# Performance work log

Measured on AMD Instinct MI355X. Metric: run time of the kernel, lower is better.

Reference implementation:

```python
import jax, jax.numpy as jnp
import numpy as np

OUTPUT_SIZE = (32, 32, 32)
TRUNCATION = (24, 24, 24)


def dct_matrix(N):
    # Orthonormal DCT-II matrix M with y_k = sum_n M[k, n] * x_n.
    n = jnp.arange(N, dtype=jnp.float32)
    k = n[:, None]
    M = jnp.cos(jnp.pi * (n[None, :] + 0.5) * k / N)
    scale = jnp.where(n == 0, jnp.sqrt(1.0 / N), jnp.sqrt(2.0 / N))
    return M * scale[:, None]


def setup_inputs() -> dict:
    key = jax.random.key(0)
    x = jax.random.normal(key, (4, 64, 64, 64, 32), dtype=jnp.float32)
    return {"x": x}


def reference(x) -> jnp.ndarray:
    # x: [B, D, H, W, C]
    B, D, H, W, C = x.shape
    t0, t1, t2 = TRUNCATION
    o0, o1, o2 = OUTPUT_SIZE

    # 3D DCT-II (ortho), separable per spatial axis.
    Md, Mh, Mw = dct_matrix(D), dct_matrix(H), dct_matrix(W)
    y = jnp.einsum('pd,bdhwc->bphwc', Md, x)
    y = jnp.einsum('qh,bphwc->bpqwc', Mh, y)
    y = jnp.einsum('rw,bpqwc->bpqrc', Mw, y)

    # Crop low frequencies, zero-pad to output size.
    y = y[:, :t0, :t1, :t2, :]
    y = jnp.pad(y, ((0, 0), (0, o0 - t0), (0, o1 - t1), (0, o2 - t2), (0, 0)))

    # 3D inverse DCT (ortho inverse = transpose of DCT matrix).
    I0, I1, I2 = dct_matrix(o0).T, dct_matrix(o1).T, dct_matrix(o2).T
    z = jnp.einsum('dp,bpqrc->bdqrc', I0, y)
    z = jnp.einsum('hq,bdqrc->bdhrc', I1, z)
    z = jnp.einsum('wr,bdhrc->bdhwc', I2, z)

    # Original module's _idct3D permutes (0,4,3,2,1) then back, which reverses
    # the spatial axis order of the output: out[b, w, h, d, c].
    return jnp.transpose(z, (0, 3, 2, 1, 4))
```

## Files before the change

kernel.cpp:

```cpp
#include <hip/hip_runtime.h>


#define PI_D 3.14159265358979323846

__global__ __launch_bounds__(256) void sp_compute_A(float* __restrict__ A) {
    int idx = blockIdx.x * 256 + threadIdx.x;
    if (idx >= 2048) return;
    int o = idx >> 6;
    int i = idx & 63;
    double acc = 0.0;
    for (int p = 0; p < 24; ++p) {
        double s32 = (p == 0) ? sqrt(1.0 / 32.0) : sqrt(2.0 / 32.0);
        double s64 = (p == 0) ? sqrt(1.0 / 64.0) : sqrt(2.0 / 64.0);
        acc += s32 * cos(PI_D * (o + 0.5) * p / 32.0)
             * s64 * cos(PI_D * (i + 0.5) * p / 64.0);
    }
    A[idx] = (float)acc;
}

template<int PASS>
__global__ __launch_bounds__(256) void sp_pass(const float* __restrict__ X,
                                               const float* __restrict__ Amat,
                                               float* __restrict__ Y) {
    __shared__ float As[2048];
    __shared__ float tiles[4][2048];

    int t = threadIdx.x;
    for (int i = t; i < 2048; i += 256) {
        int k = i >> 5, o = i & 31;
        As[i] = Amat[o * 64 + k];
    }
    __syncthreads();

    int wave = t >> 6, lane = t & 63;
    long tile = (long)blockIdx.x * 4 + wave;

    constexpr int KS = (PASS == 1) ? 32 : (PASS == 2) ? 1024 : 32768;
    constexpr int OS = (PASS == 1) ? 32 : (PASS == 2) ? 1024 : 32;

    long in_base, out_base;
    if constexpr (PASS == 1) {
        in_base  = tile * 2048;
        out_base = tile * 1024;
    } else if constexpr (PASS == 2) {
        long bd = tile >> 5; int jt = (int)tile & 31;
        in_base  = bd * 65536 + jt * 32;
        out_base = bd * 32768 + jt * 32;
    } else {
        long b = tile >> 10; int q = ((int)tile >> 5) & 31, r = (int)tile & 31;
        in_base  = b * 2097152 + q * 1024 + r * 32;
        out_base = b * 1048576 + r * 32768 + q * 1024;
    }

    float* ltile = &tiles[wave][0];
    const float* gsrc = X + in_base + (long)(lane >> 3) * KS + (lane & 7) * 4;
#pragma unroll
    for (int i = 0; i < 8; ++i) {
        __builtin_amdgcn_global_load_lds(
            (const __attribute__((address_space(1))) void*)(gsrc + (long)i * 8 * KS),
            (__attribute__((address_space(3))) void*)(ltile + i * 256),
            16, 0, 0);
    }
    asm volatile("s_waitcnt vmcnt(0)" ::: "memory");
    __builtin_amdgcn_sched_barrier(0);

    int j2 = lane & 15, og = lane >> 4;
    const float2* xs  = (const float2*)ltile + j2;
    const float4* as4 = (const float4*)As + og * 2;

    float2 acc[8];
#pragma unroll
    for (int i = 0; i < 8; ++i) acc[i] = make_float2(0.f, 0.f);

#pragma unroll
    for (int k = 0; k < 64; ++k) {
        float2 xv = xs[k * 16];
        float4 a0 = as4[k * 8];
        float4 a1 = as4[k * 8 + 1];
        acc[0].x += a0.x * xv.x; acc[0].y += a0.x * xv.y;
        acc[1].x += a0.y * xv.x; acc[1].y += a0.y * xv.y;
        acc[2].x += a0.z * xv.x; acc[2].y += a0.z * xv.y;
        acc[3].x += a0.w * xv.x; acc[3].y += a0.w * xv.y;
        acc[4].x += a1.x * xv.x; acc[4].y += a1.x * xv.y;
        acc[5].x += a1.y * xv.x; acc[5].y += a1.y * xv.y;
        acc[6].x += a1.z * xv.x; acc[6].y += a1.z * xv.y;
        acc[7].x += a1.w * xv.x; acc[7].y += a1.w * xv.y;
    }

    float2* dst = (float2*)(Y + out_base) + j2;
#pragma unroll
    for (int i = 0; i < 8; ++i) {
        int o = og * 8 + i;
        dst[(long)o * (OS / 2)] = acc[i];
    }
}

extern "C" void kernel_launch(void* const* d_in, const int* in_sizes, int n_in,
                              void* d_out, int out_size, void* d_ws, size_t ws_size,
                              hipStream_t stream) {
    const float* x = (const float*)d_in[0];
    float* out = (float*)d_out;

    float* A  = (float*)d_ws;
    float* y1 = A + 2048;
    float* y2 = y1 + 16777216;

    sp_compute_A<<<8, 256, 0, stream>>>(A);

    sp_pass<1><<<4096, 256, 0, stream>>>(x, A, y1);

    sp_pass<2><<<2048, 256, 0, stream>>>(y1, A, y2);

    sp_pass<3><<<1024, 256, 0, stream>>>(y2, A, out);
}
```

Baseline: 253.4 us.

## Double-buffer persistent tiles per wave, compute DCT matrix inline, change pass layouts

Each wave now handles several tiles, with async global-to-LDS loads double-buffered so the next tile's load overlaps the current tile's compute. The combined truncation matrix is computed in each block with cosf, which removes the separate setup kernel. The pass-2 and pass-3 index mappings are rearranged so pass-3 reads contiguously, and the register tile becomes 4x4 with float4 stores. This adds redundant per-block trig work and slightly different numerics from single-precision cos.

```diff
diff --git a/kernel.cpp b/kernel.cpp
--- a/kernel.cpp
+++ b/kernel.cpp
@@ -1,97 +1,110 @@
 #include <hip/hip_runtime.h>
 
 
-#define PI_D 3.14159265358979323846
+template<int PASS> struct Cfg;
+template<> struct Cfg<1> { static constexpr int KS = 32;   static constexpr int NT = 8; static constexpr long OS = 32;    };
+template<> struct Cfg<2> { static constexpr int KS = 1024; static constexpr int NT = 4; static constexpr long OS = 65536; };
+template<> struct Cfg<3> { static constexpr int KS = 1024; static constexpr int NT = 2; static constexpr long OS = 32;    };
 
-__global__ __launch_bounds__(256) void sp_compute_A(float* __restrict__ A) {
-    int idx = blockIdx.x * 256 + threadIdx.x;
-    if (idx >= 2048) return;
-    int o = idx >> 6;
-    int i = idx & 63;
-    double acc = 0.0;
-    for (int p = 0; p < 24; ++p) {
-        double s32 = (p == 0) ? sqrt(1.0 / 32.0) : sqrt(2.0 / 32.0);
-        double s64 = (p == 0) ? sqrt(1.0 / 64.0) : sqrt(2.0 / 64.0);
-        acc += s32 * cos(PI_D * (o + 0.5) * p / 32.0)
-             * s64 * cos(PI_D * (i + 0.5) * p / 64.0);
+template<int PASS>
+__device__ __forceinline__ void tile_bases(long tau, long& ib, long& ob) {
+    if constexpr (PASS == 1) {
+        ib = tau * 2048;
+        ob = tau * 1024;
+    } else if constexpr (PASS == 2) {
+        long bd = tau >> 5, jt = tau & 31;
+        long b = bd >> 6, d = bd & 63;
+        ib = bd * 65536 + jt * 32;
+        ob = b * 2097152 + d * 1024 + jt * 32;
+    } else {
+        long bq = tau >> 5, jt = tau & 31;
+        long b = bq >> 5, q = bq & 31;
+        ib = (b * 32 + q) * 65536 + jt * 32;
+        ob = ((b * 32 + jt) * 32 + q) * 1024;
     }
-    A[idx] = (float)acc;
 }
 
 template<int PASS>
 __global__ __launch_bounds__(256) void sp_pass(const float* __restrict__ X,
-                                               const float* __restrict__ Amat,
                                                float* __restrict__ Y) {
+    constexpr int  KS = Cfg<PASS>::KS;
+    constexpr long OS = Cfg<PASS>::OS;
+    constexpr int  NT = Cfg<PASS>::NT;
+
     __shared__ float As[2048];
-    __shared__ float tiles[4][2048];
+    __shared__ float tiles[4][2][2048];
 
     int t = threadIdx.x;
     for (int i = t; i < 2048; i += 256) {
         int k = i >> 5, o = i & 31;
-        As[i] = Amat[o * 64 + k];
+        float fo = (o + 0.5f) * (3.14159265358979f / 32.0f);
+        float fk = (k + 0.5f) * (3.14159265358979f / 64.0f);
+        float s = 0.02209708691f;
+        for (int p = 1; p < 24; ++p)
+            s += 0.04419417382f * cosf(fo * p) * cosf(fk * p);
+        As[i] = s;
     }
     __syncthreads();
 
     int wave = t >> 6, lane = t & 63;
-    long tile = (long)blockIdx.x * 4 + wave;
+    int o4 = lane >> 3, c4 = lane & 7;
+    long wg = (long)blockIdx.x * 4 + wave;
 
-    constexpr int KS = (PASS == 1) ? 32 : (PASS == 2) ? 1024 : 32768;
-    constexpr int OS = (PASS == 1) ? 32 : (PASS == 2) ? 1024 : 32;
+    float* b0 = &tiles[wave][0][0];
+    float* b1 = &tiles[wave][1][0];
 
-    long in_base, out_base;
-    if constexpr (PASS == 1) {
-        in_base  = tile * 2048;
-        out_base = tile * 1024;
-    } else if constexpr (PASS == 2) {
-        long bd = tile >> 5; int jt = (int)tile & 31;
-        in_base  = bd * 65536 + jt * 32;
-        out_base = bd * 32768 + jt * 32;
-    } else {
-        long b = tile >> 10; int q = ((int)tile >> 5) & 31, r = (int)tile & 31;
-        in_base  = b * 2097152 + q * 1024 + r * 32;
-        out_base = b * 1048576 + r * 32768 + q * 1024;
-    }
+    const float* Xl = X + (long)(lane >> 3) * KS + (lane & 7) * 4;
+    auto issue = [&](float* buf, long ib) {
+        const float* g = Xl + ib;
+#pragma unroll
+        for (int i = 0; i < 8; ++i)
+            __builtin_amdgcn_global_load_lds(
+                (const __attribute__((address_space(1))) void*)(g + (long)i * (8 * KS)),
+                (__attribute__((address_space(3))) void*)(buf + i * 256), 16, 0, 0);
+    };
 
-    float* ltile = &tiles[wave][0];
-    const float* gsrc = X + in_base + (long)(lane >> 3) * KS + (lane & 7) * 4;
+    long ib, ob;
+    tile_bases<PASS>(wg * NT + 0, ib, ob); issue(b0, ib);
+    tile_bases<PASS>(wg * NT + 1, ib, ob); issue(b1, ib);
+
+    const float4* ab = (const float4*)As;
+
+#pragma unroll 1
+    for (int i = 0; i < NT; ++i) {
+        if (i == 0)           asm volatile("s_waitcnt vmcnt(8)"  ::: "memory");
+        else if (i == NT - 1) asm volatile("s_waitcnt vmcnt(4)"  ::: "memory");
+        else                  asm volatile("s_waitcnt vmcnt(12)" ::: "memory");
+        __builtin_amdgcn_sched_barrier(0);
+
+        const float4* tb = (const float4*)((i & 1) ? b1 : b0);
+
+        float4 a0 = make_float4(0.f, 0.f, 0.f, 0.f);
+        float4 a1 = a0, a2 = a0, a3 = a0;
 #pragma unroll
-    for (int i = 0; i < 8; ++i) {
-        __builtin_amdgcn_global_load_lds(
-            (const __attribute__((address_space(1))) void*)(gsrc + (long)i * 8 * KS),
-            (__attribute__((address_space(3))) void*)(ltile + i * 256),
-            16, 0, 0);
-    }
-    asm volatile("s_waitcnt vmcnt(0)" ::: "memory");
-    __builtin_amdgcn_sched_barrier(0);
+        for (int k = 0; k < 64; ++k) {
+            float4 xv = tb[k * 8 + c4];
+            float4 av = ab[k * 8 + o4];
+            a0.x += av.x * xv.x; a0.y += av.x * xv.y; a0.z += av.x * xv.z; a0.w += av.x * xv.w;
+            a1.x += av.y * xv.x; a1.y += av.y * xv.y; a1.z += av.y * xv.z; a1.w += av.y * xv.w;
+            a2.x += av.z * xv.x; a2.y += av.z * xv.y; a2.z += av.z * xv.z; a2.w += av.z * xv.w;
+            a3.x += av.w * xv.x; a3.y += av.w * xv.y; a3.z += av.w * xv.z; a3.w += av.w * xv.w;
+        }
 
-    int j2 = lane & 15, og = lane >> 4;
-    const float2* xs  = (const float2*)ltile + j2;
-    const float4* as4 = (const float4*)As + og * 2;
+        asm volatile("s_waitcnt lgkmcnt(0)" ::: "memory");
+        __builtin_amdgcn_sched_barrier(0);
+        if (i + 2 < NT) {
+            long ibn, obn;
+            tile_bases<PASS>(wg * NT + i + 2, ibn, obn);
+            issue((i & 1) ? b1 : b0, ibn);
+        }
 
-    float2 acc[8];
-#pragma unroll
-    for (int i = 0; i < 8; ++i) acc[i] = make_float2(0.f, 0.f);
-
-#pragma unroll
-    for (int k = 0; k < 64; ++k) {
-        float2 xv = xs[k * 16];
-        float4 a0 = as4[k * 8];
-        float4 a1 = as4[k * 8 + 1];
-        acc[0].x += a0.x * xv.x; acc[0].y += a0.x * xv.y;
-        acc[1].x += a0.y * xv.x; acc[1].y += a0.y * xv.y;
-        acc[2].x += a0.z * xv.x; acc[2].y += a0.z * xv.y;
-        acc[3].x += a0.w * xv.x; acc[3].y += a0.w * xv.y;
-        acc[4].x += a1.x * xv.x; acc[4].y += a1.x * xv.y;
-        acc[5].x += a1.y * xv.x; acc[5].y += a1.y * xv.y;
-        acc[6].x += a1.z * xv.x; acc[6].y += a1.z * xv.y;
-        acc[7].x += a1.w * xv.x; acc[7].y += a1.w * xv.y;
-    }
-
-    float2* dst = (float2*)(Y + out_base) + j2;
-#pragma unroll
-    for (int i = 0; i < 8; ++i) {
-        int o = og * 8 + i;
-        dst[(long)o * (OS / 2)] = acc[i];
+        long ibc, obc;
+        tile_bases<PASS>(wg * NT + i, ibc, obc);
+        float* dst = Y + obc + (long)(o4 * 4) * OS + c4 * 4;
+        *(float4*)(dst)          = a0;
+        *(float4*)(dst + OS)     = a1;
+        *(float4*)(dst + 2 * OS) = a2;
+        *(float4*)(dst + 3 * OS) = a3;
     }
 }
 
@@ -101,15 +114,10 @@
     const float* x = (const float*)d_in[0];
     float* out = (float*)d_out;
 
-    float* A  = (float*)d_ws;
-    float* y1 = A + 2048;
+    float* y1 = (float*)d_ws;
     float* y2 = y1 + 16777216;
 
-    sp_compute_A<<<8, 256, 0, stream>>>(A);
-
-    sp_pass<1><<<4096, 256, 0, stream>>>(x, A, y1);
-
-    sp_pass<2><<<2048, 256, 0, stream>>>(y1, A, y2);
-
-    sp_pass<3><<<1024, 256, 0, stream>>>(y2, A, out);
+    sp_pass<1><<<512, 256, 0, stream>>>(x,  y1);
+    sp_pass<2><<<512, 256, 0, stream>>>(y1, y2);
+    sp_pass<3><<<512, 256, 0, stream>>>(y2, out);
 }
```

New measurement: 441.2 us. 74.1% more time.

## Fuse W and H DCT passes into one kernel and compute matrix in-kernel

Applied to the files above, without the earlier changes.

Replaces the three separable passes plus the matrix-generation kernel with two kernels. The first streams each (b,d) slab row by row through a triple-buffered LDS pipeline and applies both the W and H transforms while keeping the H accumulators in registers. The second applies the D transform as before. The combined DCT/IDCT matrix is now built per block with a Chebyshev cosine recurrence, dropping the separate launch and one full intermediate round-trip through global memory. In exchange only 256 large blocks run in the fused pass, so parallelism is lower and register pressure is high (64 matrix values plus 32 float2 accumulators per thread).

```diff
diff --git a/kernel.cpp b/kernel.cpp
--- a/kernel.cpp
+++ b/kernel.cpp
@@ -1,66 +1,111 @@
 #include <hip/hip_runtime.h>
 
 
-#define PI_D 3.14159265358979323846
-
-__global__ __launch_bounds__(256) void sp_compute_A(float* __restrict__ A) {
-    int idx = blockIdx.x * 256 + threadIdx.x;
-    if (idx >= 2048) return;
-    int o = idx >> 6;
-    int i = idx & 63;
-    double acc = 0.0;
-    for (int p = 0; p < 24; ++p) {
-        double s32 = (p == 0) ? sqrt(1.0 / 32.0) : sqrt(2.0 / 32.0);
-        double s64 = (p == 0) ? sqrt(1.0 / 64.0) : sqrt(2.0 / 64.0);
-        acc += s32 * cos(PI_D * (o + 0.5) * p / 32.0)
-             * s64 * cos(PI_D * (i + 0.5) * p / 64.0);
+__device__ __forceinline__ void fill_As(float* As) {
+    for (int i = threadIdx.x; i < 2048; i += blockDim.x) {
+        int k = i >> 5, o = i & 31;
+        double to = cos((o + 0.5) * (3.14159265358979323846 / 32.0));
+        double tk = cos((k + 0.5) * (3.14159265358979323846 / 64.0));
+        double co0 = 1.0, co1 = to, ck0 = 1.0, ck1 = tk;
+        double w2o = 2.0 * to, w2k = 2.0 * tk;
+        double s = 0.022097086912079608;
+        #pragma unroll 1
+        for (int p = 1; p < 24; ++p) {
+            s += 0.044194173824159216 * co1 * ck1;
+            double con = w2o * co1 - co0; co0 = co1; co1 = con;
+            double ckn = w2k * ck1 - ck0; ck0 = ck1; ck1 = ckn;
+        }
+        As[i] = (float)s;
     }
-    A[idx] = (float)acc;
 }
 
-template<int PASS>
-__global__ __launch_bounds__(256) void sp_pass(const float* __restrict__ X,
-                                               const float* __restrict__ Amat,
-                                               float* __restrict__ Y) {
+__global__ __launch_bounds__(512, 2) void sp_fuse_wh(const float* __restrict__ X,
+                                                     float* __restrict__ Y1) {
+    __shared__ float As[2048];
+    __shared__ float xrow[4][2048];
+
+    int t = threadIdx.x;
+    int b = blockIdx.x >> 6, d = blockIdx.x & 63;
+    const float* xbase = X + ((long)(b * 64 + d) << 17);
+
+    auto stage = [&](int h) {
+        const float* src = xbase + h * 2048 + t * 4;
+        float* dstb = &xrow[h & 3][(t >> 6) << 8];
+        __builtin_amdgcn_global_load_lds(
+            (const __attribute__((address_space(1))) void*)src,
+            (__attribute__((address_space(3))) void*)dstb, 16, 0, 0);
+    };
+
+    stage(0); stage(1); stage(2);
+    fill_As(As);
+    __syncthreads();
+
+    int r = t >> 4;
+    int c2 = t & 15;
+
+    float ar[64];
+#pragma unroll
+    for (int w = 0; w < 64; ++w) ar[w] = As[w * 32 + r];
+
+    float2 qa[32];
+#pragma unroll
+    for (int q = 0; q < 32; ++q) qa[q] = make_float2(0.f, 0.f);
+
+#pragma unroll 1
+    for (int h = 0; h < 64; ++h) {
+        if (h < 61) asm volatile("s_waitcnt vmcnt(2)" ::: "memory");
+        else        asm volatile("s_waitcnt vmcnt(0)" ::: "memory");
+        __syncthreads();
+        if (h + 3 < 64) stage(h + 3);
+
+        const float* xr = &xrow[h & 3][0];
+        float2 v = make_float2(0.f, 0.f);
+#pragma unroll
+        for (int w = 0; w < 64; ++w) {
+            float2 xv = *(const float2*)&xr[w * 32 + c2 * 2];
+            v.x += ar[w] * xv.x; v.y += ar[w] * xv.y;
+        }
+
+        const float4* ah = (const float4*)&As[h * 32];
+#pragma unroll
+        for (int qg = 0; qg < 8; ++qg) {
+            float4 a4 = ah[qg];
+            qa[qg * 4 + 0].x += a4.x * v.x; qa[qg * 4 + 0].y += a4.x * v.y;
+            qa[qg * 4 + 1].x += a4.y * v.x; qa[qg * 4 + 1].y += a4.y * v.y;
+            qa[qg * 4 + 2].x += a4.z * v.x; qa[qg * 4 + 2].y += a4.z * v.y;
+            qa[qg * 4 + 3].x += a4.w * v.x; qa[qg * 4 + 3].y += a4.w * v.y;
+        }
+    }
+
+#pragma unroll
+    for (int q = 0; q < 32; ++q) {
+        float* dst = Y1 + ((long)((b * 32 + q) * 64 + d) << 10) + r * 32 + c2 * 2;
+        *(float2*)dst = qa[q];
+    }
+}
+
+__global__ __launch_bounds__(256) void sp_pass_d(const float* __restrict__ Y1,
+                                                 float* __restrict__ Out) {
     __shared__ float As[2048];
     __shared__ float tiles[4][2048];
 
-    int t = threadIdx.x;
-    for (int i = t; i < 2048; i += 256) {
-        int k = i >> 5, o = i & 31;
-        As[i] = Amat[o * 64 + k];
-    }
+    fill_As(As);
     __syncthreads();
 
+    int t = threadIdx.x;
     int wave = t >> 6, lane = t & 63;
     long tile = (long)blockIdx.x * 4 + wave;
+    long b = tile >> 10;
+    int q = ((int)tile >> 5) & 31, r = (int)tile & 31;
 
-    constexpr int KS = (PASS == 1) ? 32 : (PASS == 2) ? 1024 : 32768;
-    constexpr int OS = (PASS == 1) ? 32 : (PASS == 2) ? 1024 : 32;
-
-    long in_base, out_base;
-    if constexpr (PASS == 1) {
-        in_base  = tile * 2048;
-        out_base = tile * 1024;
-    } else if constexpr (PASS == 2) {
-        long bd = tile >> 5; int jt = (int)tile & 31;
-        in_base  = bd * 65536 + jt * 32;
-        out_base = bd * 32768 + jt * 32;
-    } else {
-        long b = tile >> 10; int q = ((int)tile >> 5) & 31, r = (int)tile & 31;
-        in_base  = b * 2097152 + q * 1024 + r * 32;
-        out_base = b * 1048576 + r * 32768 + q * 1024;
-    }
-
+    long ib = (b * 32 + q) * 65536 + r * 32;
     float* ltile = &tiles[wave][0];
-    const float* gsrc = X + in_base + (long)(lane >> 3) * KS + (lane & 7) * 4;
+    const float* gsrc = Y1 + ib + (long)(lane >> 3) * 1024 + (lane & 7) * 4;
 #pragma unroll
-    for (int i = 0; i < 8; ++i) {
+    for (int i = 0; i < 8; ++i)
         __builtin_amdgcn_global_load_lds(
-            (const __attribute__((address_space(1))) void*)(gsrc + (long)i * 8 * KS),
-            (__attribute__((address_space(3))) void*)(ltile + i * 256),
-            16, 0, 0);
-    }
+            (const __attribute__((address_space(1))) void*)(gsrc + (long)i * 8192),
+            (__attribute__((address_space(3))) void*)(ltile + i * 256), 16, 0, 0);
     asm volatile("s_waitcnt vmcnt(0)" ::: "memory");
     __builtin_amdgcn_sched_barrier(0);
 
@@ -87,11 +132,12 @@
         acc[7].x += a1.w * xv.x; acc[7].y += a1.w * xv.y;
     }
 
-    float2* dst = (float2*)(Y + out_base) + j2;
+    long ob = ((b * 32 + r) * 32 + q) * 1024;
+    float2* dst = (float2*)(Out + ob) + j2;
 #pragma unroll
     for (int i = 0; i < 8; ++i) {
         int o = og * 8 + i;
-        dst[(long)o * (OS / 2)] = acc[i];
+        dst[o * 16] = acc[i];
     }
 }
 
@@ -100,16 +146,9 @@
                               hipStream_t stream) {
     const float* x = (const float*)d_in[0];
     float* out = (float*)d_out;
+    float* y1 = (float*)d_ws;
 
-    float* A  = (float*)d_ws;
-    float* y1 = A + 2048;
-    float* y2 = y1 + 16777216;
+    sp_fuse_wh<<<256, 512, 0, stream>>>(x, y1);
 
-    sp_compute_A<<<8, 256, 0, stream>>>(A);
-
-    sp_pass<1><<<4096, 256, 0, stream>>>(x, A, y1);
-
-    sp_pass<2><<<2048, 256, 0, stream>>>(y1, A, y2);
-
-    sp_pass<3><<<1024, 256, 0, stream>>>(y2, A, out);
+    sp_pass_d<<<1024, 256, 0, stream>>>(y1, out);
 }
```

New measurement: 297.6 us. 17.4% more time.
